# Performance work log

Measured on AMD Instinct MI355X. Metric: run time of the kernel, lower is better.

The kernel has to match this reference:

```python
import jax, jax.numpy as jnp
import numpy as np

N_NODES = 100000
N_EDGES = 1600000
D = 128


def gcn_conv(x, src, dst, ew, W, b, num_nodes):
    """PyG GCNConv: self-loops (weight 1), symmetric deg^{-1/2} normalization,
    linear transform (no bias) then scatter-add aggregation at dst, bias after."""
    loop = jnp.arange(num_nodes)
    s = jnp.concatenate([src, loop])
    d = jnp.concatenate([dst, loop])
    w = jnp.concatenate([ew, jnp.ones((num_nodes,), dtype=x.dtype)])
    deg = jax.ops.segment_sum(w, d, num_segments=num_nodes)
    dinv = jnp.where(deg > 0, jax.lax.rsqrt(deg), 0.0).astype(x.dtype)
    norm = dinv[s] * w * dinv[d]                      # [E+N]
    h = x @ W                                          # [N, out]
    msgs = h[s] * norm[:, None]                        # [E+N, out]
    return jax.ops.segment_sum(msgs, d, num_segments=num_nodes) + b


def setup_inputs() -> dict:
    key = jax.random.key(0)
    ks = jax.random.split(key, 7)
    x = jax.random.normal(ks[0], (N_NODES, D), dtype=jnp.float32)
    edge_index = jax.random.randint(ks[1], (2, N_EDGES), 0, N_NODES, dtype=jnp.int64)
    edge_weight = jax.random.uniform(ks[2], (N_EDGES,), dtype=jnp.float32)
    scale = 1.0 / np.sqrt(D)
    W1 = jax.random.normal(ks[3], (D, D), dtype=jnp.float32) * scale
    b1 = jax.random.normal(ks[4], (D,), dtype=jnp.float32) * 0.01
    W2 = jax.random.normal(ks[5], (D, D), dtype=jnp.float32) * scale
    b2 = jax.random.normal(ks[6], (D,), dtype=jnp.float32) * 0.01
    return {"x": x, "edge_index": edge_index, "edge_weight": edge_weight,
            "W1": W1, "b1": b1, "W2": W2, "b2": b2}


def reference(x, edge_index, edge_weight, W1, b1, W2, b2):
    src, dst = edge_index[0], edge_index[1]
    n = x.shape[0]
    h = gcn_conv(x, src, dst, edge_weight, W1, b1, n)
    h = jax.nn.relu(h)
    h = gcn_conv(h, src, dst, edge_weight, W2, b2, n)
    return jax.nn.relu(h)
```

## Files before the change

### kernel.cpp

```cpp
#include <hip/hip_runtime.h>

#define D 128
#define CAP 64
#define NCELL 391
#define BN2 256
#define CELLCAP 4608
#define BCAP 16
#define ABLK 768

typedef __attribute__((ext_vector_type(8))) short bf16x8;
typedef __attribute__((ext_vector_type(4))) float f32x4;
typedef __attribute__((ext_vector_type(4))) uint  u32x4;
typedef __attribute__((ext_vector_type(2))) uint  u32x2;
typedef __attribute__((ext_vector_type(2))) float f32x2;

__device__ __forceinline__ ushort f2bf(float f) {
    uint u = __float_as_uint(f);
    return (ushort)((u + 0x7FFFu + ((u >> 16) & 1u)) >> 16);
}

__global__ __launch_bounds__(256) void k_prep(const float* __restrict__ W1,
                                              const float* __restrict__ W2,
                                              ushort* __restrict__ Wt1,
                                              ushort* __restrict__ Wt2,
                                              int* scnt) {
    int i = blockIdx.x * 256 + threadIdx.x;
    if (i < NCELL) scnt[i] = 0;
    if (i < 2 * D * D) {
        const float* W = (i < D * D) ? W1 : W2;
        ushort* Wt     = (i < D * D) ? Wt1 : Wt2;
        int j = i & (D * D - 1);
        int k = j >> 7, nn = j & 127;
        Wt[nn * D + k] = f2bf(W[k * D + nn]);
    }
}

__global__ __launch_bounds__(256) void k_bin_gemm(const int* __restrict__ src,
                                                  const int* __restrict__ dst,
                                                  const float* __restrict__ ew,
                                                  int* scnt,
                                                  uint2* __restrict__ rec, int nE, int epb,
                                                  const float* __restrict__ X,
                                                  const ushort* __restrict__ Wt,
                                                  ushort* __restrict__ H, int n) {
    __shared__ __align__(16) char smem[53248];
    const int tid = threadIdx.x;

    if (blockIdx.x < ABLK) {
        uint2* lrec  = (uint2*)smem;
        int*   bcnt  = (int*)(smem + 50048);
        int*   gbase = (int*)(smem + 50048 + 1564);

        for (int i = tid; i < NCELL; i += 256) bcnt[i] = 0;
        __syncthreads();

        int e0 = blockIdx.x * epb;
        int e1 = min(e0 + epb, nE);
        for (int e = e0 + tid; e < e1; e += 256) {
            int d = dst[e];
            uint q = (uint)__float2int_rn(ew[e] * 32767.0f);
            uint2 r = make_uint2(((uint)src[e] << 15) | q, (uint)(d & (BN2 - 1)));
            int cell = d >> 8;
            int p = atomicAdd(&bcnt[cell], 1);
            if (p < BCAP) {
                lrec[cell * BCAP + p] = r;
            } else {
                int gp = atomicAdd(&scnt[cell], 1);
                if (gp < CELLCAP) rec[(size_t)cell * CELLCAP + gp] = r;
            }
        }
        __syncthreads();

        const int offs = (blockIdx.x * 97) % NCELL;

        for (int i = tid; i < NCELL; i += 256) {
            int cell = i + offs; if (cell >= NCELL) cell -= NCELL;
            int c = min(bcnt[cell], BCAP);
            gbase[cell] = (c > 0) ? atomicAdd(&scnt[cell], c) : 0;
        }
        __syncthreads();

        const int wave = tid >> 6, lane = tid & 63;
        for (int i = wave; i < NCELL; i += 4) {
            int cell = i + offs; if (cell >= NCELL) cell -= NCELL;
            int c = min(bcnt[cell], BCAP);
            if (lane < c) {
                uint2 v = lrec[cell * BCAP + lane];
                u32x2 ve = {v.x, v.y};
                __builtin_nontemporal_store(ve,
                    (u32x2*)(rec + (size_t)cell * CELLCAP + gbase[cell] + lane));
            }
        }
    } else {
        ushort (*Xs)[136] = (ushort (*)[136])smem;
        ushort (*Ws)[136] = (ushort (*)[136])(smem + 17408);
        const int row0 = (blockIdx.x - ABLK) * 64;

#pragma unroll
        for (int p = 0; p < 8; ++p) {
            int f = (p * 256 + tid) * 8;
            int nn = f >> 7, kk = f & 127;
            *(uint4*)(&Ws[nn][kk]) = *(const uint4*)(Wt + f);
        }
#pragma unroll
        for (int p = 0; p < 8; ++p) {
            int f = (p * 256 + tid) * 4;
            int r = f >> 7, kk = f & 127;
            float4 v = {0.f, 0.f, 0.f, 0.f};
            if (row0 + r < n) v = *(const float4*)(X + (size_t)(row0 + r) * D + kk);
            ushort4 o;
            o.x = f2bf(v.x); o.y = f2bf(v.y); o.z = f2bf(v.z); o.w = f2bf(v.w);
            *(ushort4*)(&Xs[r][kk]) = o;
        }
        __syncthreads();

        const int lane = tid & 63;
        const int wave = tid >> 6;
        const int m    = lane & 15;
        const int quad = lane >> 4;
        const int rw   = wave * 16;

        f32x4 acc[8] = {};
#pragma unroll
        for (int kt = 0; kt < 4; ++kt) {
            int k0 = kt * 32 + quad * 8;
            bf16x8 a = *(const bf16x8*)(&Xs[rw + m][k0]);
#pragma unroll
            for (int t = 0; t < 8; ++t) {
                bf16x8 b = *(const bf16x8*)(&Ws[t * 16 + m][k0]);
                acc[t] = __builtin_amdgcn_mfma_f32_16x16x32_bf16(a, b, acc[t], 0, 0, 0);
            }
        }

#pragma unroll
        for (int t = 0; t < 8; ++t) {
#pragma unroll
            for (int r = 0; r < 4; ++r) {
                int row = row0 + rw + quad * 4 + r;
                if (row < n) H[(size_t)row * D + t * 16 + m] = f2bf(acc[t][r]);
            }
        }
    }
}

__global__ __launch_bounds__(512) void k_build(const uint2* __restrict__ rec,
                                               const int* __restrict__ scnt,
                                               uint* __restrict__ bucket,
                                               int* __restrict__ cnt,
                                               float* __restrict__ dinv, int n) {
    __shared__ uint rows[128 * (CAP + 1)];
    __shared__ int  lcnt[128];
    const int tid  = threadIdx.x;
    const int b    = blockIdx.x >> 1;
    const int half = blockIdx.x & 1;

    if (tid < 128) lcnt[tid] = 0;
    __syncthreads();

    int c = min(scnt[b], CELLCAP);
    for (int i = tid; i < c; i += 512) {
        u32x2 r = __builtin_nontemporal_load((const u32x2*)(rec + (size_t)b * CELLCAP + i));
        int y = (int)r.y;
        if ((y >> 7) == half) {
            int nl = y & 127;
            int p = atomicAdd(&lcnt[nl], 1);
            if (p < CAP - 1) rows[nl * (CAP + 1) + p] = r.x;
        }
    }
    __syncthreads();

    if (tid < 128) {
        int node = b * BN2 + half * 128 + tid;
        int cc = min(lcnt[tid], CAP - 1);
        lcnt[tid] = cc;
        if (node < n) {
            float wsum = 0.f;
            for (int i = 0; i < cc; ++i)
                wsum += (float)(rows[tid * (CAP + 1) + i] & 32767u);
            dinv[node] = rsqrtf(1.0f + wsum * (1.0f / 32767.0f));
            cnt[node]  = cc + 1;
        }
    }
    __syncthreads();

    for (int i = tid; i < 128 * (CAP / 4); i += 512) {
        int nl  = i >> 4;
        int slb = (i & 15) << 2;
        int nd  = b * BN2 + half * 128 + nl;
        if (nd < n) {
            int ce = lcnt[nl];
            uint self = ((uint)nd << 15) | 32767u;
            u32x4 o;
#pragma unroll
            for (int k = 0; k < 4; ++k) {
                int sl = slb + k;
                uint v = 0u;
                if (sl < ce)       v = rows[nl * (CAP + 1) + sl];
                else if (sl == ce) v = self;
                o[k] = v;
            }
            *(u32x4*)(bucket + (size_t)nd * CAP + slb) = o;
        }
    }
}

__global__ __launch_bounds__(256) void k_norm(uint* __restrict__ bucket,
                                              const int* __restrict__ cnt,
                                              const float* __restrict__ dinv, int n) {
    int node = blockIdx.x * 64 + (threadIdx.x >> 2);
    if (node >= n) return;
    int lane = threadIdx.x & 3;
    float dd = dinv[node];
    int c = cnt[node];
    u32x4* row4 = (u32x4*)(bucket + (size_t)node * CAP);
    for (int u = lane; u * 4 < c; u += 4) {
        u32x4 e = row4[u];
        u32x4 o;
#pragma unroll
        for (int k = 0; k < 4; ++k) {
            uint s = e[k] >> 15;
            float w = (float)(e[k] & 32767u) * (1.0f / 32767.0f) * dinv[s] * dd;
            o[k] = (s << 15) | (uint)__float2int_rn(w * 32767.0f);
        }
        row4[u] = o;
    }
}

__global__ __launch_bounds__(256) void k_gemm_bf(const ushort* __restrict__ X,
                                                 const ushort* __restrict__ Wt,
                                                 ushort* __restrict__ H, int n) {
    __shared__ ushort Xs[64][136];
    __shared__ ushort Ws[128][136];
    const int tid  = threadIdx.x;
    const int row0 = blockIdx.x * 64;

#pragma unroll
    for (int p = 0; p < 8; ++p) {
        int f = (p * 256 + tid) * 8;
        int nn = f >> 7, kk = f & 127;
        *(uint4*)(&Ws[nn][kk]) = *(const uint4*)(Wt + f);
    }
#pragma unroll
    for (int p = 0; p < 4; ++p) {
        int f = (p * 256 + tid) * 8;
        int r = f >> 7, kk = f & 127;
        uint4 v = {0u, 0u, 0u, 0u};
        if (row0 + r < n) v = *(const uint4*)(X + (size_t)(row0 + r) * D + kk);
        *(uint4*)(&Xs[r][kk]) = v;
    }
    __syncthreads();

    const int lane = tid & 63;
    const int wave = tid >> 6;
    const int m    = lane & 15;
    const int quad = lane >> 4;
    const int rw   = wave * 16;

    f32x4 acc[8] = {};
#pragma unroll
    for (int kt = 0; kt < 4; ++kt) {
        int k0 = kt * 32 + quad * 8;
        bf16x8 a = *(const bf16x8*)(&Xs[rw + m][k0]);
#pragma unroll
        for (int t = 0; t < 8; ++t) {
            bf16x8 b = *(const bf16x8*)(&Ws[t * 16 + m][k0]);
            acc[t] = __builtin_amdgcn_mfma_f32_16x16x32_bf16(a, b, acc[t], 0, 0, 0);
        }
    }

#pragma unroll
    for (int t = 0; t < 8; ++t) {
#pragma unroll
        for (int r = 0; r < 4; ++r) {
            int row = row0 + rw + quad * 4 + r;
            if (row < n) H[(size_t)row * D + t * 16 + m] = f2bf(acc[t][r]);
        }
    }
}

template <bool OUT_BF16>
__global__ __launch_bounds__(256) void k_agg(const ushort* __restrict__ H,
                                             const int* __restrict__ cnt,
                                             const uint* __restrict__ bucket,
                                             const float* __restrict__ bias,
                                             void* __restrict__ outv, int n) {
    int node = blockIdx.x * 8 + (threadIdx.x >> 5);
    int l32  = threadIdx.x & 31;
    int nda  = min(node, n - 1);
    const uint2*  Hu2  = (const uint2*)H;
    const u32x4*  row4 = (const u32x4*)(bucket + (size_t)nda * CAP);

    int c = (node < n) ? cnt[node] : 0;
    int cmax = max(c, __shfl_xor(c, 32));

    f32x2 acc0 = {0.f, 0.f};
    f32x2 acc1 = {0.f, 0.f};
    for (int j = 0; j < cmax; j += 8) {
        u32x4 pa = __builtin_nontemporal_load(row4 + (j >> 2));
        u32x4 pb = __builtin_nontemporal_load(row4 + (j >> 2) + 1);
#pragma unroll
        for (int t = 0; t < 8; ++t) {
            uint p   = (t < 4) ? pa[t] : pb[t - 4];
            uint idx = ((p >> 10) & 0x003FFFE0u) | (uint)l32;
            uint2 h  = Hu2[idx];
            float w  = (float)(p & 32767u) * (1.0f / 32767.0f);
            f32x2 f0, f1;
            f0.x = __uint_as_float(h.x << 16);
            f0.y = __uint_as_float(h.x & 0xFFFF0000u);
            f1.x = __uint_as_float(h.y << 16);
            f1.y = __uint_as_float(h.y & 0xFFFF0000u);
            acc0 = f0 * w + acc0;
            acc1 = f1 * w + acc1;
        }
    }

    float4 bv = *(const float4*)(bias + l32 * 4);
    float r0 = fmaxf(acc0.x + bv.x, 0.f);
    float r1 = fmaxf(acc0.y + bv.y, 0.f);
    float r2 = fmaxf(acc1.x + bv.z, 0.f);
    float r3 = fmaxf(acc1.y + bv.w, 0.f);
    if (node < n) {
        if (OUT_BF16) {
            uint2 o;
            o.x = (uint)f2bf(r0) | ((uint)f2bf(r1) << 16);
            o.y = (uint)f2bf(r2) | ((uint)f2bf(r3) << 16);
            ((uint2*)outv)[(size_t)node * 32 + l32] = o;
        } else {
            f32x4 r = {r0, r1, r2, r3};
            __builtin_nontemporal_store(r, (f32x4*)outv + (size_t)node * 32 + l32);
        }
    }
}

extern "C" void kernel_launch(void* const* d_in, const int* in_sizes, int n_in,
                              void* d_out, int out_size, void* d_ws, size_t ws_size,
                              hipStream_t stream) {
    const float* x  = (const float*)d_in[0];
    const int*   ei = (const int*)d_in[1];
    const float* ew = (const float*)d_in[2];
    const float* W1 = (const float*)d_in[3];
    const float* b1 = (const float*)d_in[4];
    const float* W2 = (const float*)d_in[5];
    const float* b2 = (const float*)d_in[6];

    const int n  = in_sizes[0] / D;
    const int nE = in_sizes[2];
    const int* src = ei;
    const int* dst = ei + nE;

    float* out = (float*)d_out;

    uint2*  rec    = (uint2*)d_ws;
    uint*   bucket = (uint*)(rec + (size_t)NCELL * CELLCAP);
    ushort* Hbuf   = (ushort*)(bucket + (size_t)n * CAP);
    ushort* Abuf   = Hbuf + (size_t)n * D;
    ushort* Wt1    = Abuf + (size_t)n * D;
    ushort* Wt2    = Wt1 + D * D;
    float*  dinv   = (float*)(Wt2 + D * D);
    int*    cnt    = (int*)(dinv + n);
    int*    scnt   = cnt + n;

    const int epb      = (nE + ABLK - 1) / ABLK;
    const int nBlkAgg  = (n + 7) / 8;
    const int nBlkNorm = (n + 63) / 64;
    const int nBlkGemm = (n + 63) / 64;

    k_prep    <<<128,               256, 0, stream>>>(W1, W2, Wt1, Wt2, scnt);
    k_bin_gemm<<<ABLK + nBlkGemm,   256, 0, stream>>>(src, dst, ew, scnt, rec, nE, epb,
                                                      x, Wt1, Hbuf, n);
    k_build   <<<2 * NCELL,         512, 0, stream>>>(rec, scnt, bucket, cnt, dinv, n);
    k_norm    <<<nBlkNorm,          256, 0, stream>>>(bucket, cnt, dinv, n);

    k_agg<true>  <<<nBlkAgg,  256, 0, stream>>>(Hbuf, cnt, bucket, b1, Abuf, n);

    k_gemm_bf    <<<nBlkGemm, 256, 0, stream>>>(Abuf, Wt2, Hbuf, n);
    k_agg<false> <<<nBlkAgg,  256, 0, stream>>>(Hbuf, cnt, bucket, b2, out, n);
}
```

Measured before the change: 334.3 us.

## Fuse layer-1 aggregation with layer-2 GEMM in a single kernel

Replaces the separate layer-1 aggregation kernel and layer-2 bf16 GEMM with one kernel. Each 512-thread block gathers and aggregates 128 nodes, applies bias and ReLU, and writes the bf16 rows straight into shared memory, then multiplies them by W2 with MFMA. This removes the global-memory write and re-read of the intermediate activation and one kernel launch. In exchange, each block holds about 70KB of LDS and runs the latency-bound gather loop serially over 8 iterations, which cuts occupancy for the gather phase.

```diff
diff --git a/kernel.cpp b/kernel.cpp
--- a/kernel.cpp
+++ b/kernel.cpp
@@ -226,27 +226,64 @@
     }
 }
 
-__global__ __launch_bounds__(256) void k_gemm_bf(const ushort* __restrict__ X,
-                                                 const ushort* __restrict__ Wt,
-                                                 ushort* __restrict__ H, int n) {
-    __shared__ ushort Xs[64][136];
+__global__ __launch_bounds__(512) void k_agg_gemm(const ushort* __restrict__ H,
+                                                  const int* __restrict__ cnt,
+                                                  const uint* __restrict__ bucket,
+                                                  const float* __restrict__ bias,
+                                                  const ushort* __restrict__ Wt,
+                                                  ushort* __restrict__ Hout, int n) {
+    __shared__ ushort Xs[128][136];
     __shared__ ushort Ws[128][136];
     const int tid  = threadIdx.x;
-    const int row0 = blockIdx.x * 64;
-
-#pragma unroll
-    for (int p = 0; p < 8; ++p) {
-        int f = (p * 256 + tid) * 8;
+    const int row0 = blockIdx.x * 128;
+
+#pragma unroll
+    for (int p = 0; p < 4; ++p) {
+        int f = (p * 512 + tid) * 8;
         int nn = f >> 7, kk = f & 127;
         *(uint4*)(&Ws[nn][kk]) = *(const uint4*)(Wt + f);
     }
-#pragma unroll
-    for (int p = 0; p < 4; ++p) {
-        int f = (p * 256 + tid) * 8;
-        int r = f >> 7, kk = f & 127;
-        uint4 v = {0u, 0u, 0u, 0u};
-        if (row0 + r < n) v = *(const uint4*)(X + (size_t)(row0 + r) * D + kk);
-        *(uint4*)(&Xs[r][kk]) = v;
+
+    const int l32 = tid & 31;
+    const uint2* Hu2 = (const uint2*)H;
+    for (int it = 0; it < 8; ++it) {
+        int lr   = it * 16 + (tid >> 5);
+        int node = row0 + lr;
+        int nda  = min(node, n - 1);
+        const u32x4* row4 = (const u32x4*)(bucket + (size_t)nda * CAP);
+        int c = (node < n) ? cnt[node] : 0;
+        int cmax = max(c, __shfl_xor(c, 32));
+
+        f32x2 acc0 = {0.f, 0.f};
+        f32x2 acc1 = {0.f, 0.f};
+        for (int j = 0; j < cmax; j += 8) {
+            u32x4 pa = __builtin_nontemporal_load(row4 + (j >> 2));
+            u32x4 pb = __builtin_nontemporal_load(row4 + (j >> 2) + 1);
+#pragma unroll
+            for (int t = 0; t < 8; ++t) {
+                uint p   = (t < 4) ? pa[t] : pb[t - 4];
+                uint idx = ((p >> 10) & 0x003FFFE0u) | (uint)l32;
+                uint2 h  = Hu2[idx];
+                float w  = (float)(p & 32767u) * (1.0f / 32767.0f);
+                f32x2 f0, f1;
+                f0.x = __uint_as_float(h.x << 16);
+                f0.y = __uint_as_float(h.x & 0xFFFF0000u);
+                f1.x = __uint_as_float(h.y << 16);
+                f1.y = __uint_as_float(h.y & 0xFFFF0000u);
+                acc0 = f0 * w + acc0;
+                acc1 = f1 * w + acc1;
+            }
+        }
+
+        float4 bv = *(const float4*)(bias + l32 * 4);
+        float r0 = fmaxf(acc0.x + bv.x, 0.f);
+        float r1 = fmaxf(acc0.y + bv.y, 0.f);
+        float r2 = fmaxf(acc1.x + bv.z, 0.f);
+        float r3 = fmaxf(acc1.y + bv.w, 0.f);
+        uint2 o;
+        o.x = (uint)f2bf(r0) | ((uint)f2bf(r1) << 16);
+        o.y = (uint)f2bf(r2) | ((uint)f2bf(r3) << 16);
+        *(uint2*)(&Xs[lr][l32 * 4]) = o;
     }
     __syncthreads();
 
@@ -273,7 +310,7 @@
 #pragma unroll
         for (int r = 0; r < 4; ++r) {
             int row = row0 + rw + quad * 4 + r;
-            if (row < n) H[(size_t)row * D + t * 16 + m] = f2bf(acc[t][r]);
+            if (row < n) Hout[(size_t)row * D + t * 16 + m] = f2bf(acc[t][r]);
         }
     }
 }
@@ -364,6 +401,7 @@
     const int nBlkAgg  = (n + 7) / 8;
     const int nBlkNorm = (n + 63) / 64;
     const int nBlkGemm = (n + 63) / 64;
+    const int nBlkFuse = (n + 127) / 128;
 
     k_prep    <<<128,               256, 0, stream>>>(W1, W2, Wt1, Wt2, scnt);
     k_bin_gemm<<<ABLK + nBlkGemm,   256, 0, stream>>>(src, dst, ew, scnt, rec, nE, epb,
@@ -371,8 +409,7 @@
     k_build   <<<2 * NCELL,         512, 0, stream>>>(rec, scnt, bucket, cnt, dinv, n);
     k_norm    <<<nBlkNorm,          256, 0, stream>>>(bucket, cnt, dinv, n);
 
-    k_agg<true>  <<<nBlkAgg,  256, 0, stream>>>(Hbuf, cnt, bucket, b1, Abuf, n);
-
-    k_gemm_bf    <<<nBlkGemm, 256, 0, stream>>>(Abuf, Wt2, Hbuf, n);
-    k_agg<false> <<<nBlkAgg,  256, 0, stream>>>(Hbuf, cnt, bucket, b2, out, n);
-}
+    k_agg_gemm<<<nBlkFuse, 512, 0, stream>>>(Hbuf, cnt, bucket, b1, Wt2, Abuf, n);
+
+    k_agg<false> <<<nBlkAgg, 256, 0, stream>>>(Abuf, cnt, bucket, b2, out, n);
+}
```

Measured after the change: 339.0 us. Within noise of the previous version (+1.4%).
